# Optimization experiments

Measured on AMD Instinct MI355X. Metric: run time of the kernel, lower is better.

Reference implementation:

```python
import jax, jax.numpy as jnp
import numpy as np

N_NODES = 10000
N_EDGES = 60000
D = 128          # latent_size
L = 15           # num_layers
EPS = 1e-5       # LayerNorm eps (torch default)


def _layernorm(h, g, b):
    mu = jnp.mean(h, axis=-1, keepdims=True)
    var = jnp.mean(jnp.square(h - mu), axis=-1, keepdims=True)
    return (h - mu) * jax.lax.rsqrt(var + EPS) * g + b


def _mlp(h, w1, b1, g1, bt1, w2, b2, g2, bt2):
    # Linear -> LayerNorm -> GELU(exact) -> [Dropout: identity in eval] -> Linear -> LayerNorm
    h = _layernorm(h @ w1 + b1, g1, bt1)
    h = jax.nn.gelu(h, approximate=False)
    return _layernorm(h @ w2 + b2, g2, bt2)


def setup_inputs() -> dict:
    key = jax.random.key(0)
    ks = jax.random.split(key, 20)
    x = jax.random.normal(ks[0], (N_NODES, D), dtype=jnp.float32)
    edge_index = jax.random.randint(ks[1], (2, N_EDGES), 0, N_NODES, dtype=jnp.int32)
    edge_attr = jax.random.normal(ks[2], (N_EDGES, D), dtype=jnp.float32)
    s = 0.02
    # Edge MLP params: Linear(3D->2D), LN(2D), Linear(2D->D), LN(D), stacked over L layers
    ew1 = jax.random.normal(ks[3], (L, 3 * D, 2 * D), dtype=jnp.float32) * s
    eb1 = jnp.zeros((L, 2 * D), dtype=jnp.float32)
    eg1 = jnp.ones((L, 2 * D), dtype=jnp.float32)
    ebt1 = jnp.zeros((L, 2 * D), dtype=jnp.float32)
    ew2 = jax.random.normal(ks[4], (L, 2 * D, D), dtype=jnp.float32) * s
    eb2 = jnp.zeros((L, D), dtype=jnp.float32)
    eg2 = jnp.ones((L, D), dtype=jnp.float32)
    ebt2 = jnp.zeros((L, D), dtype=jnp.float32)
    # Node MLP params: Linear(2D->2D), LN(2D), Linear(2D->D), LN(D)
    nw1 = jax.random.normal(ks[5], (L, 2 * D, 2 * D), dtype=jnp.float32) * s
    nb1 = jnp.zeros((L, 2 * D), dtype=jnp.float32)
    ng1 = jnp.ones((L, 2 * D), dtype=jnp.float32)
    nbt1 = jnp.zeros((L, 2 * D), dtype=jnp.float32)
    nw2 = jax.random.normal(ks[6], (L, 2 * D, D), dtype=jnp.float32) * s
    nb2 = jnp.zeros((L, D), dtype=jnp.float32)
    ng2 = jnp.ones((L, D), dtype=jnp.float32)
    nbt2 = jnp.zeros((L, D), dtype=jnp.float32)
    return dict(x=x, edge_index=edge_index, edge_attr=edge_attr,
                ew1=ew1, eb1=eb1, eg1=eg1, ebt1=ebt1, ew2=ew2, eb2=eb2, eg2=eg2, ebt2=ebt2,
                nw1=nw1, nb1=nb1, ng1=ng1, nbt1=nbt1, nw2=nw2, nb2=nb2, ng2=ng2, nbt2=nbt2)


def reference(x, edge_index, edge_attr,
              ew1, eb1, eg1, ebt1, ew2, eb2, eg2, ebt2,
              nw1, nb1, ng1, nbt1, nw2, nb2, ng2, nbt2):
    row, col = edge_index[0], edge_index[1]
    # neighbor counts (per destination node), clamped to >= 1; constant across layers
    count = jax.ops.segment_sum(jnp.ones((edge_index.shape[1],), dtype=x.dtype), col,
                                num_segments=x.shape[0])
    count = jnp.maximum(count, 1.0)[:, None]  # [N,1]
    for i in range(L):
        edge_input = jnp.concatenate([x[row], x[col], edge_attr], axis=1)  # [E, 3D]
        edge_attr = edge_attr + _mlp(edge_input, ew1[i], eb1[i], eg1[i], ebt1[i],
                                     ew2[i], eb2[i], eg2[i], ebt2[i])
        agg = jax.ops.segment_sum(edge_attr, col, num_segments=x.shape[0]) / count  # [N, D]
        node_input = jnp.concatenate([x, agg], axis=1)  # [N, 2D]
        x = x + _mlp(node_input, nw1[i], nb1[i], ng1[i], nbt1[i],
                     nw2[i], nb2[i], ng2[i], nbt2[i])
    return x, edge_attr
```

## Files before the change

### kernel.cpp

```cpp
#include <hip/hip_runtime.h>
#include <hip/hip_bf16.h>
#include <math.h>

#define NN 10000
#define NE 60000
#define DD 128
#define NL 15
#define LN_EPS 1e-5f

typedef __attribute__((ext_vector_type(8))) short short8;
typedef __attribute__((ext_vector_type(4))) float floatx4;

__device__ __forceinline__ unsigned short f2bf(float f) {
    unsigned u = __float_as_uint(f);
    u += 0x7fff + ((u >> 16) & 1);
    return (unsigned short)(u >> 16);
}
__device__ __forceinline__ unsigned bc2(float a, float b) {
    __hip_bfloat162 t = __float22bfloat162_rn(make_float2(a, b));
    return *(unsigned*)&t;
}
__device__ __forceinline__ float bfl(unsigned w) { return __uint_as_float(w << 16); }
__device__ __forceinline__ float bfh(unsigned w) { return __uint_as_float(w & 0xffff0000u); }
__device__ __forceinline__ float gelu_fast(float y) {
    float u = y * y;
    float s2 = y * fmaf(u, 0.07135481283f, 1.59576912161f);
    return y * __builtin_amdgcn_rcpf(1.0f + __expf(-s2));
}

__device__ __forceinline__ void pack_one(const float* __restrict__ W, unsigned short* __restrict__ P,
                                         int u, int Kk, int Nk, bool perm) {
    int per_layer = Kk * Nk;
    int i = u / per_layer;
    int v0 = u - i * per_layer;
    int S = Kk >> 5;
    int t = v0 / (S * 512);
    int rem = v0 - t * (S * 512);
    int s = rem >> 9;
    int v = rem & 511;
    int l = v >> 3, j = v & 7;
    int kv = (s << 5) + ((l >> 4) << 3) + j;
    int k = perm ? (((kv & 15) << 4) | (kv >> 4)) : kv;
    int n = (t << 4) + (l & 15);
    P[u] = f2bf(W[((size_t)i * Kk + k) * Nk + n]);
}

#define N_EW1 (NL * 384 * 256)
#define N_EW2 (NL * 256 * 128)
#define N_NW1 (NL * 256 * 256)
#define N_NW2 (NL * 256 * 128)

__global__ void pack_all(const float* __restrict__ ew1, const float* __restrict__ ew2,
                         const float* __restrict__ nw1, const float* __restrict__ nw2,
                         unsigned short* __restrict__ P) {
    int tid = blockIdx.x * blockDim.x + threadIdx.x;
    if (tid < N_EW1) { pack_one(ew1, P, tid, 384, 256, false); return; }
    tid -= N_EW1;
    if (tid < N_EW2) { pack_one(ew2, P + N_EW1, tid, 256, 128, true); return; }
    tid -= N_EW2;
    if (tid < N_NW1) { pack_one(nw1, P + N_EW1 + N_EW2, tid, 256, 256, false); return; }
    tid -= N_NW1;
    if (tid < N_NW2) { pack_one(nw2, P + N_EW1 + N_EW2 + N_NW1, tid, 256, 128, true); return; }
}

__global__ void hist_kernel(const int* __restrict__ ecol, int* __restrict__ cnt) {
    int e = blockIdx.x * blockDim.x + threadIdx.x;
    if (e < NE) atomicAdd(&cnt[ecol[e]], 1);
}

__global__ void scan_kernel(const int* __restrict__ cnt, int* __restrict__ starts,
                            int* __restrict__ cursor, float* __restrict__ cinv) {
    __shared__ int part[256];
    int t = threadIdx.x;
    const int chunk = (NN + 255) / 256;
    int lo = t * chunk;
    int hi = lo + chunk; if (hi > NN) hi = NN;
    int s = 0;
    for (int n = lo; n < hi; ++n) s += cnt[n];
    part[t] = s;
    __syncthreads();
    for (int off = 1; off < 256; off <<= 1) {
        int v = (t >= off) ? part[t - off] : 0;
        __syncthreads();
        part[t] += v;
        __syncthreads();
    }
    int base = part[t] - s;
    for (int n = lo; n < hi; ++n) {
        int c = cnt[n];
        starts[n] = base; cursor[n] = base;
        cinv[n] = 1.0f / (float)(c > 0 ? c : 1);
        base += c;
    }
}

__global__ void fill_kernel(const int* __restrict__ erow, const int* __restrict__ ecol,
                            int* __restrict__ cursor, int* __restrict__ eidx,
                            int* __restrict__ erow_s, int* __restrict__ ecol_s) {
    int e = blockIdx.x * blockDim.x + threadIdx.x;
    if (e < NE) {
        int c = ecol[e];
        int slot = atomicAdd(&cursor[c], 1);
        eidx[slot] = e;
        erow_s[slot] = erow[e];
        ecol_s[slot] = c;
    }
}

__global__ void init_shadow(const float* __restrict__ x, const float* __restrict__ ea,
                            const int* __restrict__ eidx,
                            unsigned short* __restrict__ xb, unsigned short* __restrict__ eb) {
    int t = blockIdx.x * blockDim.x + threadIdx.x;
    const int NX = NN * DD / 4;
    const int NEA = NE * DD / 4;
    if (t < NX) {
        float4 v = *(const float4*)&x[(size_t)t * 4];
        uint2 p; p.x = bc2(v.x, v.y); p.y = bc2(v.z, v.w);
        *(uint2*)&xb[(size_t)t * 4] = p;
    } else if (t < NX + NEA) {
        size_t u = (size_t)(t - NX);
        int slot = (int)(u >> 5);
        int j = (int)(u & 31);
        int e = eidx[slot];
        float4 v = *(const float4*)&ea[(size_t)e * DD + j * 4];
        uint2 p; p.x = bc2(v.x, v.y); p.y = bc2(v.z, v.w);
        *(uint2*)&eb[u * 4] = p;
    }
}

template <int K1, int ROWS_TOTAL, bool EDGE>
__global__ __launch_bounds__(256, 4)
void mlp_mfma(const unsigned short* __restrict__ xb16,
              const int* __restrict__ erow, const int* __restrict__ ecol,
              const unsigned short* __restrict__ eas16,
              const int* __restrict__ starts, const int* __restrict__ cnt,
              const float* __restrict__ cinv,
              const int* __restrict__ eidx,
              float* __restrict__ target,
              unsigned short* __restrict__ shadow,
              const unsigned short* __restrict__ W1p, const unsigned short* __restrict__ W2p,
              const float* __restrict__ b1, const float* __restrict__ g1, const float* __restrict__ bt1,
              const float* __restrict__ b2, const float* __restrict__ g2, const float* __restrict__ bt2)
{
    constexpr int S1 = K1 / 32;
    constexpr int ROWS = 32;
    __shared__ union {
        unsigned short a1[ROWS * K1];
        unsigned short h[ROWS * 256];
    } sm;
    __shared__ float red1[ROWS][8];
    __shared__ float red2[ROWS][8];

    const int tid  = threadIdx.x;
    const int lane = tid & 63;
    const int w    = tid >> 6;
    const int q    = lane >> 4;
    const int c15  = lane & 15;
    const int r0   = blockIdx.x * ROWS;

    const int qn = w & 3;
    const int np = w & 3;

    {
        const int r = tid >> 3;
        const int g = tid & 7;
        const int row_g = r0 + r;
        const bool ok = (ROWS_TOTAL % ROWS == 0) || (row_g < ROWS_TOTAL);
        const int rg = ok ? row_g : 0;
        if constexpr (EDGE) {
            const unsigned short* baseA = &xb16[(size_t)erow[rg] * DD];
            const unsigned short* baseB = &xb16[(size_t)ecol[rg] * DD];
            const unsigned short* baseC = &eas16[(size_t)rg * DD];
            #pragma unroll
            for (int it = 0; it < 6; ++it) {
                const int gg = g + 8 * it;
                const int p = gg << 3;
                const unsigned short* src = (p < 128) ? (baseA + p)
                                          : (p < 256) ? (baseB + (p - 128))
                                                      : (baseC + (p - 256));
                uint4 v = *(const uint4*)src;
                *(uint4*)&sm.a1[r * K1 + ((gg ^ (r & 7)) << 3)] = v;
            }
        } else {
            const unsigned short* baseA = &xb16[(size_t)rg * DD];
            #pragma unroll
            for (int it = 0; it < 2; ++it) {
                const int gg = g + 8 * it;
                uint4 v = *(const uint4*)(baseA + (gg << 3));
                *(uint4*)&sm.a1[r * K1 + ((gg ^ (r & 7)) << 3)] = v;
            }
            const int st = starts[rg];
            const int de = cnt[rg];
            const float ci = cinv[rg];
            float4 sa0 = {0.f,0.f,0.f,0.f}, sa1 = sa0, sb0 = sa0, sb1 = sa0;
            const unsigned short* er = &eas16[(size_t)st * DD + (g << 3)];
            for (int i = 0; i < de; ++i, er += DD) {
                uint4 a = *(const uint4*)er;
                uint4 b = *(const uint4*)(er + 64);
                sa0.x += bfl(a.x); sa0.y += bfh(a.x); sa0.z += bfl(a.y); sa0.w += bfh(a.y);
                sa1.x += bfl(a.z); sa1.y += bfh(a.z); sa1.z += bfl(a.w); sa1.w += bfh(a.w);
                sb0.x += bfl(b.x); sb0.y += bfh(b.x); sb0.z += bfl(b.y); sb0.w += bfh(b.y);
                sb1.x += bfl(b.z); sb1.y += bfh(b.z); sb1.z += bfl(b.w); sb1.w += bfh(b.w);
            }
            uint4 v;
            v.x = bc2(sa0.x * ci, sa0.y * ci); v.y = bc2(sa0.z * ci, sa0.w * ci);
            v.z = bc2(sa1.x * ci, sa1.y * ci); v.w = bc2(sa1.z * ci, sa1.w * ci);
            const int gg2 = g + 16;
            *(uint4*)&sm.a1[r * K1 + ((gg2 ^ (r & 7)) << 3)] = v;
            v.x = bc2(sb0.x * ci, sb0.y * ci); v.y = bc2(sb0.z * ci, sb0.w * ci);
            v.z = bc2(sb1.x * ci, sb1.y * ci); v.w = bc2(sb1.z * ci, sb1.w * ci);
            const int gg3 = g + 24;
            *(uint4*)&sm.a1[r * K1 + ((gg3 ^ (r & 7)) << 3)] = v;
        }
    }
    __syncthreads();

    float b2c[2], g2c[2], t2c[2];
    #pragma unroll
    for (int jn = 0; jn < 2; ++jn) {
        int col = (((np << 1) + jn) << 4) + c15;
        b2c[jn] = b2[col]; g2c[jn] = g2[col]; t2c[jn] = bt2[col];
    }

    floatx4 acc[2][4];
    #pragma unroll
    for (int mt = 0; mt < 2; ++mt)
        #pragma unroll
        for (int ntl = 0; ntl < 4; ++ntl)
            acc[mt][ntl] = (floatx4){0.f, 0.f, 0.f, 0.f};

    __builtin_amdgcn_s_setprio(1);
    #pragma unroll
    for (int s = 0; s < S1; ++s) {
        short8 af[2];
        #pragma unroll
        for (int mt = 0; mt < 2; ++mt) {
            int row  = (mt << 4) + c15;
            int kgrp = ((s << 2) + q) ^ (row & 7);
            af[mt] = *(const short8*)&sm.a1[row * K1 + (kgrp << 3)];
        }
        #pragma unroll
        for (int ntl = 0; ntl < 4; ++ntl) {
            const short8 bf = *(const short8*)&W1p[((((((qn << 2) + ntl) * S1) + s) << 6) + lane) << 3];
            #pragma unroll
            for (int mt = 0; mt < 2; ++mt)
                acc[mt][ntl] = __builtin_amdgcn_mfma_f32_16x16x32_bf16(af[mt], bf, acc[mt][ntl], 0, 0, 0);
        }
    }
    __builtin_amdgcn_s_setprio(0);

    float tpre[2][4][2];
    if constexpr (EDGE) {
        #pragma unroll
        for (int jm = 0; jm < 2; ++jm)
            #pragma unroll
            for (int r = 0; r < 4; ++r) {
                int row = (jm << 4) + (q << 2) + r;
                #pragma unroll
                for (int jn = 0; jn < 2; ++jn) {
                    int col = (((np << 1) + jn) << 4) + c15;
                    int vc = 256 + col;
                    int addr = row * K1 + ((((vc >> 3) ^ (row & 7)) << 3) | (vc & 7));
                    tpre[jm][r][jn] = __uint_as_float((unsigned)sm.a1[addr] << 16);
                }
            }
    }

    float b1c[4], g1c[4], t1c[4];
    #pragma unroll
    for (int ntl = 0; ntl < 4; ++ntl) {
        int col = (((qn << 2) + ntl) << 4) + c15;
        b1c[ntl] = b1[col]; g1c[ntl] = g1[col]; t1c[ntl] = bt1[col];
    }
    #pragma unroll
    for (int mt = 0; mt < 2; ++mt)
        #pragma unroll
        for (int r = 0; r < 4; ++r) {
            float p = 0.f, sq = 0.f;
            #pragma unroll
            for (int ntl = 0; ntl < 4; ++ntl) {
                float v = acc[mt][ntl][r] + b1c[ntl];
                acc[mt][ntl][r] = v;
                p += v; sq += v * v;
            }
            p += __shfl_xor(p, 1);  sq += __shfl_xor(sq, 1);
            p += __shfl_xor(p, 2);  sq += __shfl_xor(sq, 2);
            p += __shfl_xor(p, 4);  sq += __shfl_xor(sq, 4);
            p += __shfl_xor(p, 8);  sq += __shfl_xor(sq, 8);
            if (c15 == 0) {
                int row = (mt << 4) + (q << 2) + r;
                red1[row][(qn << 1) + 0] = p;
                red1[row][(qn << 1) + 1] = sq;
            }
        }
    __syncthreads();

    #pragma unroll
    for (int mt = 0; mt < 2; ++mt)
        #pragma unroll
        for (int r = 0; r < 4; ++r) {
            int row = (mt << 4) + (q << 2) + r;
            const float4 p0 = *(const float4*)&red1[row][0];
            const float4 p1 = *(const float4*)&red1[row][4];
            float p  = p0.x + p0.z + p1.x + p1.z;
            float sq = p0.y + p0.w + p1.y + p1.w;
            float mu = p * (1.0f / 256.0f);
            float rs = rsqrtf(sq * (1.0f / 256.0f) - mu * mu + LN_EPS);
            float y0 = gelu_fast((acc[mt][0][r] - mu) * rs * g1c[0] + t1c[0]);
            float y1 = gelu_fast((acc[mt][1][r] - mu) * rs * g1c[1] + t1c[1]);
            float y2 = gelu_fast((acc[mt][2][r] - mu) * rs * g1c[2] + t1c[2]);
            float y3 = gelu_fast((acc[mt][3][r] - mu) * rs * g1c[3] + t1c[3]);
            uint2 hp;
            hp.x = bc2(y0, y1);
            hp.y = bc2(y2, y3);
            int gg = (c15 << 1) + (qn >> 1);
            int addr = row * 256 + (((gg ^ (row & 7)) << 3) | ((qn & 1) << 2));
            *(uint2*)&sm.h[addr] = hp;
        }
    __syncthreads();

    floatx4 acc2[2][2];
    #pragma unroll
    for (int jm = 0; jm < 2; ++jm)
        #pragma unroll
        for (int jn = 0; jn < 2; ++jn)
            acc2[jm][jn] = (floatx4){0.f, 0.f, 0.f, 0.f};

    __builtin_amdgcn_s_setprio(1);
    #pragma unroll
    for (int s = 0; s < 8; ++s) {
        short8 a2[2];
        #pragma unroll
        for (int jm = 0; jm < 2; ++jm) {
            int mrow = (jm << 4) + c15;
            int kgrp = ((s << 2) + q) ^ (mrow & 7);
            a2[jm] = *(const short8*)&sm.h[mrow * 256 + (kgrp << 3)];
        }
        #pragma unroll
        for (int jn = 0; jn < 2; ++jn) {
            int nt = (np << 1) + jn;
            const short8 b = *(const short8*)&W2p[((((nt << 3) + s) << 6) + lane) << 3];
            #pragma unroll
            for (int jm = 0; jm < 2; ++jm)
                acc2[jm][jn] = __builtin_amdgcn_mfma_f32_16x16x32_bf16(a2[jm], b, acc2[jm][jn], 0, 0, 0);
        }
    }
    __builtin_amdgcn_s_setprio(0);

    if constexpr (!EDGE) {
        #pragma unroll
        for (int jm = 0; jm < 2; ++jm)
            #pragma unroll
            for (int r = 0; r < 4; ++r) {
                int row = (jm << 4) + (q << 2) + r;
                int rowg = r0 + row;
                const bool okk = (ROWS_TOTAL % ROWS == 0) || (rowg < ROWS_TOTAL);
                const int rgs = okk ? rowg : 0;
                #pragma unroll
                for (int jn = 0; jn < 2; ++jn) {
                    int col = (((np << 1) + jn) << 4) + c15;
                    tpre[jm][r][jn] = target[(size_t)rgs * DD + col];
                }
            }
    }

    #pragma unroll
    for (int jm = 0; jm < 2; ++jm)
        #pragma unroll
        for (int r = 0; r < 4; ++r) {
            float p = 0.f, sq = 0.f;
            #pragma unroll
            for (int jn = 0; jn < 2; ++jn) {
                float v = acc2[jm][jn][r] + b2c[jn];
                acc2[jm][jn][r] = v;
                p += v; sq += v * v;
            }
            p += __shfl_xor(p, 1);  sq += __shfl_xor(sq, 1);
            p += __shfl_xor(p, 2);  sq += __shfl_xor(sq, 2);
            p += __shfl_xor(p, 4);  sq += __shfl_xor(sq, 4);
            p += __shfl_xor(p, 8);  sq += __shfl_xor(sq, 8);
            if (c15 == 0) {
                int row = (jm << 4) + (q << 2) + r;
                red2[row][(np << 1) + 0] = p;
                red2[row][(np << 1) + 1] = sq;
            }
        }
    __syncthreads();

    #pragma unroll
    for (int jm = 0; jm < 2; ++jm)
        #pragma unroll
        for (int r = 0; r < 4; ++r) {
            int row = (jm << 4) + (q << 2) + r;
            const float4 pp0 = *(const float4*)&red2[row][0];
            const float4 pp1 = *(const float4*)&red2[row][4];
            float p  = pp0.x + pp0.z + pp1.x + pp1.z;
            float sq = pp0.y + pp0.w + pp1.y + pp1.w;
            float mu = p * (1.0f / 128.0f);
            float rs = rsqrtf(sq * (1.0f / 128.0f) - mu * mu + LN_EPS);
            int rowg = r0 + row;
            const bool okk = (ROWS_TOTAL % ROWS == 0) || (rowg < ROWS_TOTAL);
            #pragma unroll
            for (int jn = 0; jn < 2; ++jn) {
                int col = (((np << 1) + jn) << 4) + c15;
                float o = (acc2[jm][jn][r] - mu) * rs * g2c[jn] + t2c[jn];
                float t = tpre[jm][r][jn] + o;
                if constexpr (EDGE) {
                    int oaddr = row * 128 + ((((col >> 3) ^ (row & 7)) << 3) | (col & 7));
                    sm.h[oaddr] = f2bf(t);
                    if (target) {
                        int orig = eidx[rowg];
                        target[(size_t)orig * DD + col] = t;
                    }
                } else {
                    if (okk) {
                        target[(size_t)rowg * DD + col] = t;
                        shadow[(size_t)rowg * DD + col] = f2bf(t);
                    }
                }
            }
        }

    if constexpr (EDGE) {
        __syncthreads();
        #pragma unroll
        for (int k = 0; k < 2; ++k) {
            int c = tid + (k << 8);
            int row = c >> 4;
            int G = c & 15;
            uint4 v = *(const uint4*)&sm.h[row * 128 + ((G ^ (row & 7)) << 3)];
            *(uint4*)&shadow[(size_t)(r0 + row) * DD + (G << 3)] = v;
        }
    }
}

extern "C" void kernel_launch(void* const* d_in, const int* in_sizes, int n_in,
                              void* d_out, int out_size, void* d_ws, size_t ws_size,
                              hipStream_t stream) {
    const float* x_in  = (const float*)d_in[0];
    const int*   ei    = (const int*)  d_in[1];
    const float* ea_in = (const float*)d_in[2];
    const float* ew1 = (const float*)d_in[3];
    const float* eb1 = (const float*)d_in[4];
    const float* eg1 = (const float*)d_in[5];
    const float* ebt1= (const float*)d_in[6];
    const float* ew2 = (const float*)d_in[7];
    const float* eb2 = (const float*)d_in[8];
    const float* eg2 = (const float*)d_in[9];
    const float* ebt2= (const float*)d_in[10];
    const float* nw1 = (const float*)d_in[11];
    const float* nb1 = (const float*)d_in[12];
    const float* ng1 = (const float*)d_in[13];
    const float* nbt1= (const float*)d_in[14];
    const float* nw2 = (const float*)d_in[15];
    const float* nb2 = (const float*)d_in[16];
    const float* ng2 = (const float*)d_in[17];
    const float* nbt2= (const float*)d_in[18];

    const int* erow = ei;
    const int* ecol = ei + NE;

    float* xbuf  = (float*)d_out;
    float* eabuf = (float*)d_out + NN * DD;

    unsigned short* ew1p  = (unsigned short*)d_ws;
    unsigned short* ew2p  = ew1p + N_EW1;
    unsigned short* nw1p  = ew2p + N_EW2;
    unsigned short* nw2p  = nw1p + N_NW1;
    unsigned short* xb16  = nw2p + N_NW2;
    unsigned short* eas16 = xb16 + (size_t)NN * DD;
    int*   cnt    = (int*)(eas16 + (size_t)NE * DD);
    int*   starts = cnt + NN;
    int*   cursor = starts + NN;
    int*   eidx   = cursor + NN;
    int*   erow_s = eidx + NE;
    int*   ecol_s = erow_s + NE;
    float* cinv   = (float*)(ecol_s + NE);

    hipMemcpyAsync(xbuf, x_in, (size_t)NN * DD * sizeof(float), hipMemcpyDeviceToDevice, stream);

    hipMemsetAsync(cnt, 0, NN * sizeof(int), stream);
    hist_kernel<<<(NE + 255) / 256, 256, 0, stream>>>(ecol, cnt);
    scan_kernel<<<1, 256, 0, stream>>>(cnt, starts, cursor, cinv);
    fill_kernel<<<(NE + 255) / 256, 256, 0, stream>>>(erow, ecol, cursor, eidx, erow_s, ecol_s);

    {
        int ntot = (NN * DD + NE * DD) / 4;
        init_shadow<<<(ntot + 255) / 256, 256, 0, stream>>>(x_in, ea_in, eidx, xb16, eas16);
    }

    {
        int ntot = N_EW1 + N_EW2 + N_NW1 + N_NW2;
        pack_all<<<(ntot + 255) / 256, 256, 0, stream>>>(ew1, ew2, nw1, nw2, ew1p);
    }

    for (int i = 0; i < NL; ++i) {
        mlp_mfma<384, NE, true><<<NE / 32, 256, 0, stream>>>(
            xb16, erow_s, ecol_s, eas16, nullptr, nullptr, nullptr, eidx,
            (i == NL - 1) ? eabuf : nullptr, eas16,
            ew1p + (size_t)i * 384 * 256, ew2p + (size_t)i * 256 * 128,
            eb1 + (size_t)i * 256, eg1 + (size_t)i * 256, ebt1 + (size_t)i * 256,
            eb2 + (size_t)i * 128, eg2 + (size_t)i * 128, ebt2 + (size_t)i * 128);
        mlp_mfma<256, NN, false><<<(NN + 31) / 32, 256, 0, stream>>>(
            xb16, nullptr, nullptr, eas16, starts, cnt, cinv, nullptr,
            xbuf, xb16,
            nw1p + (size_t)i * 256 * 256, nw2p + (size_t)i * 256 * 128,
            nb1 + (size_t)i * 256, ng1 + (size_t)i * 256, nbt1 + (size_t)i * 256,
            nb2 + (size_t)i * 128, ng2 + (size_t)i * 128, nbt2 + (size_t)i * 128);
    }
}
```

Measured before the change: 1.104 ms.

## Split edge MLP into dedicated 64-row, 512-thread kernel with 8-wave tiling

Adds a dedicated edge-MLP kernel that processes 64 edges per block with 8 waves instead of 32 edges with 4 waves. Each wave now owns two 16-column tiles of the first GEMM and one of the second, and reuses each weight fragment across four row tiles. This halves weight fragment loads per edge and raises MFMA work per global weight read. The node kernel is split out unchanged. The cost is a larger LDS footprint (~48KB a1 union) and more registers per wave, which may lower occupancy.

```diff
diff --git a/kernel.cpp b/kernel.cpp
--- a/kernel.cpp
+++ b/kernel.cpp
@@ -128,14 +128,227 @@
     }
 }
 
-template <int K1, int ROWS_TOTAL, bool EDGE>
+__global__ __launch_bounds__(512, 4)
+void mlp_edge64(const unsigned short* __restrict__ xb16,
+                const int* __restrict__ erow, const int* __restrict__ ecol,
+                const unsigned short* __restrict__ eas16,
+                const int* __restrict__ eidx,
+                float* __restrict__ target,
+                unsigned short* __restrict__ shadow,
+                const unsigned short* __restrict__ W1p, const unsigned short* __restrict__ W2p,
+                const float* __restrict__ b1, const float* __restrict__ g1, const float* __restrict__ bt1,
+                const float* __restrict__ b2, const float* __restrict__ g2, const float* __restrict__ bt2)
+{
+    constexpr int K1 = 384, S1 = 12, ROWS = 64;
+    __shared__ union {
+        unsigned short a1[ROWS * K1];
+        unsigned short h[ROWS * 256];
+    } sm;
+    __shared__ float red1[ROWS][16];
+    __shared__ float red2[ROWS][16];
+
+    const int tid  = threadIdx.x;
+    const int lane = tid & 63;
+    const int w    = tid >> 6;
+    const int q    = lane >> 4;
+    const int c15  = lane & 15;
+    const int r0   = blockIdx.x * ROWS;
+
+    {
+        const int r = tid >> 3;
+        const int g = tid & 7;
+        const int row_g = r0 + r;
+        const int rg = (row_g < NE) ? row_g : 0;
+        const unsigned short* baseA = &xb16[(size_t)erow[rg] * DD];
+        const unsigned short* baseB = &xb16[(size_t)ecol[rg] * DD];
+        const unsigned short* baseC = &eas16[(size_t)rg * DD];
+        #pragma unroll
+        for (int it = 0; it < 6; ++it) {
+            const int gg = g + 8 * it;
+            const int p = gg << 3;
+            const unsigned short* src = (p < 128) ? (baseA + p)
+                                      : (p < 256) ? (baseB + (p - 128))
+                                                  : (baseC + (p - 256));
+            uint4 v = *(const uint4*)src;
+            *(uint4*)&sm.a1[r * K1 + ((gg ^ (r & 7)) << 3)] = v;
+        }
+    }
+    __syncthreads();
+
+    const int col2 = (w << 4) + c15;
+    float b2c = b2[col2], g2c = g2[col2], t2c = bt2[col2];
+
+    floatx4 acc[4][2];
+    #pragma unroll
+    for (int mt = 0; mt < 4; ++mt)
+        #pragma unroll
+        for (int jn = 0; jn < 2; ++jn)
+            acc[mt][jn] = (floatx4){0.f, 0.f, 0.f, 0.f};
+
+    __builtin_amdgcn_s_setprio(1);
+    #pragma unroll
+    for (int s = 0; s < S1; ++s) {
+        short8 af[4];
+        #pragma unroll
+        for (int mt = 0; mt < 4; ++mt) {
+            int row  = (mt << 4) + c15;
+            int kgrp = ((s << 2) + q) ^ (row & 7);
+            af[mt] = *(const short8*)&sm.a1[row * K1 + (kgrp << 3)];
+        }
+        #pragma unroll
+        for (int jn = 0; jn < 2; ++jn) {
+            const short8 bf = *(const short8*)&W1p[(((((w << 1) + jn) * S1 + s) << 6) + lane) << 3];
+            #pragma unroll
+            for (int mt = 0; mt < 4; ++mt)
+                acc[mt][jn] = __builtin_amdgcn_mfma_f32_16x16x32_bf16(af[mt], bf, acc[mt][jn], 0, 0, 0);
+        }
+    }
+    __builtin_amdgcn_s_setprio(0);
+
+    float tpre[4][4];
+    #pragma unroll
+    for (int jm = 0; jm < 4; ++jm)
+        #pragma unroll
+        for (int r = 0; r < 4; ++r) {
+            int row = (jm << 4) + (q << 2) + r;
+            int vc = 256 + col2;
+            int addr = row * K1 + ((((vc >> 3) ^ (row & 7)) << 3) | (vc & 7));
+            tpre[jm][r] = __uint_as_float((unsigned)sm.a1[addr] << 16);
+        }
+
+    float b1c[2], g1c[2], t1c[2];
+    #pragma unroll
+    for (int jn = 0; jn < 2; ++jn) {
+        int col = (((w << 1) + jn) << 4) + c15;
+        b1c[jn] = b1[col]; g1c[jn] = g1[col]; t1c[jn] = bt1[col];
+    }
+    #pragma unroll
+    for (int mt = 0; mt < 4; ++mt)
+        #pragma unroll
+        for (int r = 0; r < 4; ++r) {
+            float v0 = acc[mt][0][r] + b1c[0]; acc[mt][0][r] = v0;
+            float v1 = acc[mt][1][r] + b1c[1]; acc[mt][1][r] = v1;
+            float p = v0 + v1;
+            float sq = fmaf(v0, v0, v1 * v1);
+            p += __shfl_xor(p, 1);  sq += __shfl_xor(sq, 1);
+            p += __shfl_xor(p, 2);  sq += __shfl_xor(sq, 2);
+            p += __shfl_xor(p, 4);  sq += __shfl_xor(sq, 4);
+            p += __shfl_xor(p, 8);  sq += __shfl_xor(sq, 8);
+            if (c15 == 0) {
+                int row = (mt << 4) + (q << 2) + r;
+                red1[row][(w << 1) + 0] = p;
+                red1[row][(w << 1) + 1] = sq;
+            }
+        }
+    __syncthreads();
+
+    const int qnp = w >> 1;
+    const int hh  = w & 1;
+    #pragma unroll
+    for (int mt = 0; mt < 4; ++mt)
+        #pragma unroll
+        for (int r = 0; r < 4; ++r) {
+            int row = (mt << 4) + (q << 2) + r;
+            const float4 p0 = *(const float4*)&red1[row][0];
+            const float4 p1 = *(const float4*)&red1[row][4];
+            const float4 p2 = *(const float4*)&red1[row][8];
+            const float4 p3 = *(const float4*)&red1[row][12];
+            float p  = p0.x + p0.z + p1.x + p1.z + p2.x + p2.z + p3.x + p3.z;
+            float sq = p0.y + p0.w + p1.y + p1.w + p2.y + p2.w + p3.y + p3.w;
+            float mu = p * (1.0f / 256.0f);
+            float rs = rsqrtf(sq * (1.0f / 256.0f) - mu * mu + LN_EPS);
+            float y0 = gelu_fast((acc[mt][0][r] - mu) * rs * g1c[0] + t1c[0]);
+            float y1 = gelu_fast((acc[mt][1][r] - mu) * rs * g1c[1] + t1c[1]);
+            unsigned hp = bc2(y0, y1);
+            int gg = (c15 << 1) + (qnp >> 1);
+            int addr = row * 256 + (((gg ^ (row & 7)) << 3) | ((qnp & 1) << 2) | (hh << 1));
+            *(unsigned*)&sm.h[addr] = hp;
+        }
+    __syncthreads();
+
+    floatx4 acc2[4];
+    #pragma unroll
+    for (int jm = 0; jm < 4; ++jm) acc2[jm] = (floatx4){0.f, 0.f, 0.f, 0.f};
+
+    __builtin_amdgcn_s_setprio(1);
+    #pragma unroll
+    for (int s = 0; s < 8; ++s) {
+        short8 a2[4];
+        #pragma unroll
+        for (int jm = 0; jm < 4; ++jm) {
+            int mrow = (jm << 4) + c15;
+            int kgrp = ((s << 2) + q) ^ (mrow & 7);
+            a2[jm] = *(const short8*)&sm.h[mrow * 256 + (kgrp << 3)];
+        }
+        const short8 b = *(const short8*)&W2p[((((w << 3) + s) << 6) + lane) << 3];
+        #pragma unroll
+        for (int jm = 0; jm < 4; ++jm)
+            acc2[jm] = __builtin_amdgcn_mfma_f32_16x16x32_bf16(a2[jm], b, acc2[jm], 0, 0, 0);
+    }
+    __builtin_amdgcn_s_setprio(0);
+
+    #pragma unroll
+    for (int jm = 0; jm < 4; ++jm)
+        #pragma unroll
+        for (int r = 0; r < 4; ++r) {
+            float v = acc2[jm][r] + b2c;
+            acc2[jm][r] = v;
+            float p = v, sq = v * v;
+            p += __shfl_xor(p, 1);  sq += __shfl_xor(sq, 1);
+            p += __shfl_xor(p, 2);  sq += __shfl_xor(sq, 2);
+            p += __shfl_xor(p, 4);  sq += __shfl_xor(sq, 4);
+            p += __shfl_xor(p, 8);  sq += __shfl_xor(sq, 8);
+            if (c15 == 0) {
+                int row = (jm << 4) + (q << 2) + r;
+                red2[row][(w << 1) + 0] = p;
+                red2[row][(w << 1) + 1] = sq;
+            }
+        }
+    __syncthreads();
+
+    #pragma unroll
+    for (int jm = 0; jm < 4; ++jm)
+        #pragma unroll
+        for (int r = 0; r < 4; ++r) {
+            int row = (jm << 4) + (q << 2) + r;
+            const float4 p0 = *(const float4*)&red2[row][0];
+            const float4 p1 = *(const float4*)&red2[row][4];
+            const float4 p2 = *(const float4*)&red2[row][8];
+            const float4 p3 = *(const float4*)&red2[row][12];
+            float p  = p0.x + p0.z + p1.x + p1.z + p2.x + p2.z + p3.x + p3.z;
+            float sq = p0.y + p0.w + p1.y + p1.w + p2.y + p2.w + p3.y + p3.w;
+            float mu = p * (1.0f / 128.0f);
+            float rs = rsqrtf(sq * (1.0f / 128.0f) - mu * mu + LN_EPS);
+            float o = (acc2[jm][r] - mu) * rs * g2c + t2c;
+            float t = tpre[jm][r] + o;
+            int oaddr = row * 128 + ((((col2 >> 3) ^ (row & 7)) << 3) | (col2 & 7));
+            sm.h[oaddr] = f2bf(t);
+            int rowg = r0 + row;
+            if (target && rowg < NE) {
+                int orig = eidx[rowg];
+                target[(size_t)orig * DD + col2] = t;
+            }
+        }
+    __syncthreads();
+
+    #pragma unroll
+    for (int k = 0; k < 2; ++k) {
+        int c = tid + (k << 9);
+        int row = c >> 4;
+        int G = c & 15;
+        if (r0 + row < NE) {
+            uint4 v = *(const uint4*)&sm.h[row * 128 + ((G ^ (row & 7)) << 3)];
+            *(uint4*)&shadow[(size_t)(r0 + row) * DD + (G << 3)] = v;
+        }
+    }
+}
+
+template <int K1, int ROWS_TOTAL>
 __global__ __launch_bounds__(256, 4)
-void mlp_mfma(const unsigned short* __restrict__ xb16,
-              const int* __restrict__ erow, const int* __restrict__ ecol,
+void mlp_node(const unsigned short* __restrict__ xb16,
               const unsigned short* __restrict__ eas16,
               const int* __restrict__ starts, const int* __restrict__ cnt,
               const float* __restrict__ cinv,
-              const int* __restrict__ eidx,
               float* __restrict__ target,
               unsigned short* __restrict__ shadow,
               const unsigned short* __restrict__ W1p, const unsigned short* __restrict__ W2p,
@@ -167,51 +380,35 @@
         const int row_g = r0 + r;
         const bool ok = (ROWS_TOTAL % ROWS == 0) || (row_g < ROWS_TOTAL);
         const int rg = ok ? row_g : 0;
-        if constexpr (EDGE) {
-            const unsigned short* baseA = &xb16[(size_t)erow[rg] * DD];
-            const unsigned short* baseB = &xb16[(size_t)ecol[rg] * DD];
-            const unsigned short* baseC = &eas16[(size_t)rg * DD];
-            #pragma unroll
-            for (int it = 0; it < 6; ++it) {
-                const int gg = g + 8 * it;
-                const int p = gg << 3;
-                const unsigned short* src = (p < 128) ? (baseA + p)
-                                          : (p < 256) ? (baseB + (p - 128))
-                                                      : (baseC + (p - 256));
-                uint4 v = *(const uint4*)src;
-                *(uint4*)&sm.a1[r * K1 + ((gg ^ (r & 7)) << 3)] = v;
-            }
-        } else {
-            const unsigned short* baseA = &xb16[(size_t)rg * DD];
-            #pragma unroll
-            for (int it = 0; it < 2; ++it) {
-                const int gg = g + 8 * it;
-                uint4 v = *(const uint4*)(baseA + (gg << 3));
-                *(uint4*)&sm.a1[r * K1 + ((gg ^ (r & 7)) << 3)] = v;
-            }
-            const int st = starts[rg];
-            const int de = cnt[rg];
-            const float ci = cinv[rg];
-            float4 sa0 = {0.f,0.f,0.f,0.f}, sa1 = sa0, sb0 = sa0, sb1 = sa0;
-            const unsigned short* er = &eas16[(size_t)st * DD + (g << 3)];
-            for (int i = 0; i < de; ++i, er += DD) {
-                uint4 a = *(const uint4*)er;
-                uint4 b = *(const uint4*)(er + 64);
-                sa0.x += bfl(a.x); sa0.y += bfh(a.x); sa0.z += bfl(a.y); sa0.w += bfh(a.y);
-                sa1.x += bfl(a.z); sa1.y += bfh(a.z); sa1.z += bfl(a.w); sa1.w += bfh(a.w);
-                sb0.x += bfl(b.x); sb0.y += bfh(b.x); sb0.z += bfl(b.y); sb0.w += bfh(b.y);
-                sb1.x += bfl(b.z); sb1.y += bfh(b.z); sb1.z += bfl(b.w); sb1.w += bfh(b.w);
-            }
-            uint4 v;
-            v.x = bc2(sa0.x * ci, sa0.y * ci); v.y = bc2(sa0.z * ci, sa0.w * ci);
-            v.z = bc2(sa1.x * ci, sa1.y * ci); v.w = bc2(sa1.z * ci, sa1.w * ci);
-            const int gg2 = g + 16;
-            *(uint4*)&sm.a1[r * K1 + ((gg2 ^ (r & 7)) << 3)] = v;
-            v.x = bc2(sb0.x * ci, sb0.y * ci); v.y = bc2(sb0.z * ci, sb0.w * ci);
-            v.z = bc2(sb1.x * ci, sb1.y * ci); v.w = bc2(sb1.z * ci, sb1.w * ci);
-            const int gg3 = g + 24;
-            *(uint4*)&sm.a1[r * K1 + ((gg3 ^ (r & 7)) << 3)] = v;
-        }
+        const unsigned short* baseA = &xb16[(size_t)rg * DD];
+        #pragma unroll
+        for (int it = 0; it < 2; ++it) {
+            const int gg = g + 8 * it;
+            uint4 v = *(const uint4*)(baseA + (gg << 3));
+            *(uint4*)&sm.a1[r * K1 + ((gg ^ (r & 7)) << 3)] = v;
+        }
+        const int st = starts[rg];
+        const int de = cnt[rg];
+        const float ci = cinv[rg];
+        float4 sa0 = {0.f,0.f,0.f,0.f}, sa1 = sa0, sb0 = sa0, sb1 = sa0;
+        const unsigned short* er = &eas16[(size_t)st * DD + (g << 3)];
+        for (int i = 0; i < de; ++i, er += DD) {
+            uint4 a = *(const uint4*)er;
+            uint4 b = *(const uint4*)(er + 64);
+            sa0.x += bfl(a.x); sa0.y += bfh(a.x); sa0.z += bfl(a.y); sa0.w += bfh(a.y);
+            sa1.x += bfl(a.z); sa1.y += bfh(a.z); sa1.z += bfl(a.w); sa1.w += bfh(a.w);
+            sb0.x += bfl(b.x); sb0.y += bfh(b.x); sb0.z += bfl(b.y); sb0.w += bfh(b.y);
+            sb1.x += bfl(b.z); sb1.y += bfh(b.z); sb1.z += bfl(b.w); sb1.w += bfh(b.w);
+        }
+        uint4 v;
+        v.x = bc2(sa0.x * ci, sa0.y * ci); v.y = bc2(sa0.z * ci, sa0.w * ci);
+        v.z = bc2(sa1.x * ci, sa1.y * ci); v.w = bc2(sa1.z * ci, sa1.w * ci);
+        const int gg2 = g + 16;
+        *(uint4*)&sm.a1[r * K1 + ((gg2 ^ (r & 7)) << 3)] = v;
+        v.x = bc2(sb0.x * ci, sb0.y * ci); v.y = bc2(sb0.z * ci, sb0.w * ci);
+        v.z = bc2(sb1.x * ci, sb1.y * ci); v.w = bc2(sb1.z * ci, sb1.w * ci);
+        const int gg3 = g + 24;
+        *(uint4*)&sm.a1[r * K1 + ((gg3 ^ (r & 7)) << 3)] = v;
     }
     __syncthreads();
 
@@ -248,23 +445,6 @@
         }
     }
     __builtin_amdgcn_s_setprio(0);
-
-    float tpre[2][4][2];
-    if constexpr (EDGE) {
-        #pragma unroll
-        for (int jm = 0; jm < 2; ++jm)
-            #pragma unroll
-            for (int r = 0; r < 4; ++r) {
-                int row = (jm << 4) + (q << 2) + r;
-                #pragma unroll
-                for (int jn = 0; jn < 2; ++jn) {
-                    int col = (((np << 1) + jn) << 4) + c15;
-                    int vc = 256 + col;
-                    int addr = row * K1 + ((((vc >> 3) ^ (row & 7)) << 3) | (vc & 7));
-                    tpre[jm][r][jn] = __uint_as_float((unsigned)sm.a1[addr] << 16);
-                }
-            }
-    }
 
     float b1c[4], g1c[4], t1c[4];
     #pragma unroll
@@ -347,22 +527,21 @@
     }
     __builtin_amdgcn_s_setprio(0);
 
-    if constexpr (!EDGE) {
-        #pragma unroll
-        for (int jm = 0; jm < 2; ++jm)
+    float tpre[2][4][2];
+    #pragma unroll
+    for (int jm = 0; jm < 2; ++jm)
+        #pragma unroll
+        for (int r = 0; r < 4; ++r) {
+            int row = (jm << 4) + (q << 2) + r;
+            int rowg = r0 + row;
+            const bool okk = (ROWS_TOTAL % ROWS == 0) || (rowg < ROWS_TOTAL);
+            const int rgs = okk ? rowg : 0;
             #pragma unroll
-            for (int r = 0; r < 4; ++r) {
-                int row = (jm << 4) + (q << 2) + r;
-                int rowg = r0 + row;
-                const bool okk = (ROWS_TOTAL % ROWS == 0) || (rowg < ROWS_TOTAL);
-                const int rgs = okk ? rowg : 0;
-                #pragma unroll
-                for (int jn = 0; jn < 2; ++jn) {
-                    int col = (((np << 1) + jn) << 4) + c15;
-                    tpre[jm][r][jn] = target[(size_t)rgs * DD + col];
-                }
-            }
-    }
+            for (int jn = 0; jn < 2; ++jn) {
+                int col = (((np << 1) + jn) << 4) + c15;
+                tpre[jm][r][jn] = target[(size_t)rgs * DD + col];
+            }
+        }
 
     #pragma unroll
     for (int jm = 0; jm < 2; ++jm)
@@ -405,33 +584,12 @@
                 int col = (((np << 1) + jn) << 4) + c15;
                 float o = (acc2[jm][jn][r] - mu) * rs * g2c[jn] + t2c[jn];
                 float t = tpre[jm][r][jn] + o;
-                if constexpr (EDGE) {
-                    int oaddr = row * 128 + ((((col >> 3) ^ (row & 7)) << 3) | (col & 7));
-                    sm.h[oaddr] = f2bf(t);
-                    if (target) {
-                        int orig = eidx[rowg];
-                        target[(size_t)orig * DD + col] = t;
-                    }
-                } else {
-                    if (okk) {
-                        target[(size_t)rowg * DD + col] = t;
-                        shadow[(size_t)rowg * DD + col] = f2bf(t);
-                    }
+                if (okk) {
+                    target[(size_t)rowg * DD + col] = t;
+                    shadow[(size_t)rowg * DD + col] = f2bf(t);
                 }
             }
         }
-
-    if constexpr (EDGE) {
-        __syncthreads();
-        #pragma unroll
-        for (int k = 0; k < 2; ++k) {
-            int c = tid + (k << 8);
-            int row = c >> 4;
-            int G = c & 15;
-            uint4 v = *(const uint4*)&sm.h[row * 128 + ((G ^ (row & 7)) << 3)];
-            *(uint4*)&shadow[(size_t)(r0 + row) * DD + (G << 3)] = v;
-        }
-    }
 }
 
 extern "C" void kernel_launch(void* const* d_in, const int* in_sizes, int n_in,
@@ -495,14 +653,14 @@
     }
 
     for (int i = 0; i < NL; ++i) {
-        mlp_mfma<384, NE, true><<<NE / 32, 256, 0, stream>>>(
-            xb16, erow_s, ecol_s, eas16, nullptr, nullptr, nullptr, eidx,
+        mlp_edge64<<<(NE + 63) / 64, 512, 0, stream>>>(
+            xb16, erow_s, ecol_s, eas16, eidx,
             (i == NL - 1) ? eabuf : nullptr, eas16,
             ew1p + (size_t)i * 384 * 256, ew2p + (size_t)i * 256 * 128,
             eb1 + (size_t)i * 256, eg1 + (size_t)i * 256, ebt1 + (size_t)i * 256,
             eb2 + (size_t)i * 128, eg2 + (size_t)i * 128, ebt2 + (size_t)i * 128);
-        mlp_mfma<256, NN, false><<<(NN + 31) / 32, 256, 0, stream>>>(
-            xb16, nullptr, nullptr, eas16, starts, cnt, cinv, nullptr,
+        mlp_node<256, NN><<<(NN + 31) / 32, 256, 0, stream>>>(
+            xb16, eas16, starts, cnt, cinv,
             xbuf, xb16,
             nw1p + (size_t)i * 256 * 256, nw2p + (size_t)i * 256 * 128,
             nb1 + (size_t)i * 256, ng1 + (size_t)i * 256, nbt1 + (size_t)i * 256,
```

Result: slower. 1.416 ms (+28.3%).
